# Performance work log

Measured on AMD Instinct MI355X. Metric: run time of the kernel, lower is better.

## Reference

```python
import jax, jax.numpy as jnp
import numpy as np

SPLINE_ORDER = 3
GRID_SIZE = 1
# efficient-kan style grid over [-1,1], extended by spline_order on each side; h = 2/grid_size = 2
GRID = jnp.arange(-SPLINE_ORDER, GRID_SIZE + SPLINE_ORDER + 1, dtype=jnp.float32) * 2.0 - 1.0
NB = GRID_SIZE + SPLINE_ORDER  # 4 basis functions per input feature
EPS = 1e-5


def b_splines(x, grid):
    # x: [..., in] -> [..., in, NB] via Cox-de Boor recursion
    xe = x[..., None]
    b = ((xe >= grid[:-1]) & (xe < grid[1:])).astype(x.dtype)
    for p in range(1, SPLINE_ORDER + 1):
        b = ((xe - grid[:-(p + 1)]) / (grid[p:-1] - grid[:-(p + 1)]) * b[..., :-1]
             + (grid[p + 1:] - xe) / (grid[p + 1:] - grid[1:-p]) * b[..., 1:])
    return b


def kan_linear(x, base_w, spline_w):
    # base branch: silu(x) @ W_base^T ; spline branch: B(x) contracted with W_spline [out,in,NB]
    base = jnp.einsum('...i,oi->...o', jax.nn.silu(x), base_w)
    sp = jnp.einsum('...ik,oik->...o', b_splines(x, GRID), spline_w)
    return base + sp


def kan_conv2x2(x, base_w, spline_w):
    # x: [B,C,H,W] -> [B,C_out,H-1,W-1]
    p = jax.lax.conv_general_dilated_patches(x, (2, 2), (1, 1), 'VALID')  # [B, C*4, H', W']
    p = jnp.moveaxis(p, 1, -1)  # [B,H',W',C*4]
    y = kan_linear(p, base_w, spline_w)  # [B,H',W',C_out]
    return jnp.moveaxis(y, -1, 1)


def bn2d(x, g, b):
    m = x.mean((0, 2, 3), keepdims=True)
    v = x.var((0, 2, 3), keepdims=True)
    return (x - m) * jax.lax.rsqrt(v + EPS) * g[None, :, None, None] + b[None, :, None, None]


def bn1d(x, g, b):
    m = x.mean(0, keepdims=True)
    v = x.var(0, keepdims=True)
    return (x - m) * jax.lax.rsqrt(v + EPS) * g[None, :] + b[None, :]


def maxpool2(x):
    B, C, H, W = x.shape
    Hc, Wc = (H // 2) * 2, (W // 2) * 2
    return x[:, :, :Hc, :Wc].reshape(B, C, H // 2, 2, W // 2, 2).max((3, 5))


def setup_inputs() -> dict:
    key = jax.random.key(0)
    ks = jax.random.split(key, 16)
    f32 = jnp.float32
    d = {
        'x': jax.random.normal(ks[0], (1024, 3, 32, 32), f32),
        'base_w1': jax.random.normal(ks[1], (32, 12), f32) * 0.2,
        'spline_w1': jax.random.normal(ks[2], (32, 12, NB), f32) * 0.1,
        'bn1_g': jnp.ones((32,), f32), 'bn1_b': jnp.zeros((32,), f32),
        'base_w2': jax.random.normal(ks[3], (64, 128), f32) * 0.08,
        'spline_w2': jax.random.normal(ks[4], (64, 128, NB), f32) * 0.04,
        'bn2_g': jnp.ones((64,), f32), 'bn2_b': jnp.zeros((64,), f32),
        'fc1_w': jax.random.normal(ks[5], (64, 3136), f32) * 0.02,
        'fc1_b': jnp.zeros((64,), f32),
        'bn3_g': jnp.ones((64,), f32), 'bn3_b': jnp.zeros((64,), f32),
        'fc2_w': jax.random.normal(ks[6], (10, 64), f32) * 0.1,
        'fc2_b': jnp.zeros((10,), f32),
    }
    return d


def reference(x, base_w1, spline_w1, bn1_g, bn1_b, base_w2, spline_w2, bn2_g, bn2_b,
              fc1_w, fc1_b, bn3_g, bn3_b, fc2_w, fc2_b):
    h = kan_conv2x2(x, base_w1, spline_w1)            # [B,32,31,31]
    h = jax.nn.relu(bn2d(h, bn1_g, bn1_b))
    h = maxpool2(h)                                   # [B,32,15,15]
    h = kan_conv2x2(h, base_w2, spline_w2)            # [B,64,14,14]
    h = jax.nn.relu(bn2d(h, bn2_g, bn2_b))
    h = maxpool2(h)                                   # [B,64,7,7]
    h = h.reshape(h.shape[0], -1)                     # [B,3136]
    h = h @ fc1_w.T + fc1_b
    h = jax.nn.relu(bn1d(h, bn3_g, bn3_b))
    # Dropout is identity at inference
    return h @ fc2_w.T + fc2_b                        # [B,10]
```

## Files before the change

kernel.cpp:

```cpp
#include <hip/hip_runtime.h>
#include <math.h>

#define BN_EPS 1e-5f

typedef __attribute__((ext_vector_type(8))) _Float16 f16x8;
typedef __attribute__((ext_vector_type(4))) _Float16 f16x4;
typedef __attribute__((ext_vector_type(2))) __fp16 fp16v2;
typedef __attribute__((ext_vector_type(4))) float f32x4;


__device__ __forceinline__ float siluf(float v) {
    return v * __builtin_amdgcn_rcpf(1.0f + __expf(-v));
}

__device__ __forceinline__ void expand5(float v, float f[5]) {
    f[0] = siluf(v);
    float u = (v + 7.0f) * 0.5f;
#pragma unroll
    for (int i = 0; i < 4; ++i) {
        float a = fabsf(u - (float)(i + 2));
        float p = fmaxf(2.0f - a, 0.0f);
        float q = fmaxf(1.0f - a, 0.0f);
        f[i + 1] = p * p * p - 4.0f * (q * q * q);
    }
}

__device__ __forceinline__ int pkh(float a, float b) {
    union { fp16v2 h2; int i; } u;
    u.h2 = __builtin_amdgcn_cvt_pkrtz(a, b);
    return u.i;
}


__global__ __launch_bounds__(256) void prep_kernel(
        const float* __restrict__ fw1, unsigned int* __restrict__ wTh2,
        const float* __restrict__ bw2, const float* __restrict__ sw2,
        _Float16* __restrict__ Wf,
        const float* __restrict__ bw1, const float* __restrict__ sw1,
        _Float16* __restrict__ Wf1) {
    int blk = blockIdx.x;
    if (blk < 392) {
        int t = blk * 256 + threadIdx.x;
        int o = t & 63;
        int j2 = t >> 6;
        int jc = (j2 * 2) & 63;
        int q2 = (j2 * 2) >> 6;
        wTh2[t] = (unsigned int)pkh(fw1[(size_t)o * 3136 + jc * 49 + q2],
                                    fw1[(size_t)o * 3136 + (jc + 1) * 49 + q2]);
    } else if (blk < 552) {
        int t = (blk - 392) * 256 + threadIdx.x;
        if (t >= 64 * 640) return;
        int n = t / 640;
        int k = t - n * 640;
        int s = k / 160;
        int r = k - s * 160;
        int f = r >> 5;
        int c = r & 31;
        float val = (f == 0) ? bw2[n * 128 + c * 4 + s]
                             : sw2[n * 512 + c * 16 + s * 4 + (f - 1)] * (1.0f / 6.0f);
        Wf[t] = (_Float16)val;
    } else {
        int t = (blk - 552) * 256 + threadIdx.x;
        if (t >= 32 * 64) return;
        int n = t >> 6;
        int k = t & 63;
        int s = k >> 4, j = k & 15;
        float val = 0.f;
        if (j < 15) {
            int f = j / 3, c = j - f * 3;
            int i = c * 4 + s;
            val = (f == 0) ? bw1[n * 12 + i]
                           : sw1[(n * 12 + i) * 4 + f - 1] * (1.0f / 6.0f);
        }
        Wf1[t] = (_Float16)val;
    }
}


__global__ __launch_bounds__(256, 4) void conv1_kernel(
        const float* __restrict__ x, const _Float16* __restrict__ Wf1,
        _Float16* __restrict__ pooled, float* __restrict__ part) {
    __shared__ _Float16 Eu[1025 * 16];
    __shared__ float Rs[4][64];
    char* EuB = (char*)Eu;

    int t = threadIdx.x;
    int lane = t & 63, wv = t >> 6;
    int quad = lane >> 4, l15 = lane & 15;
    int b = blockIdx.x;

    const _Float16* wb0 = Wf1 + (size_t)l15 * 64 + quad * 8;
    f16x8 bf00 = *(const f16x8*)(wb0);
    f16x8 bf01 = *(const f16x8*)(wb0 + 32);
    f16x8 bf10 = *(const f16x8*)(wb0 + 16 * 64);
    f16x8 bf11 = *(const f16x8*)(wb0 + 16 * 64 + 32);

    float xv[12];
    const float* xb = x + (size_t)b * 3072;
#pragma unroll
    for (int k = 0; k < 12; ++k) xv[k] = xb[t + k * 256];
#pragma unroll
    for (int k = 0; k < 12; ++k) {
        int idx = t + k * 256;
        int c = idx >> 10;
        int pos = idx & 1023;
        float f[5];
        expand5(xv[k], f);
        int rb = pos * 32;
        int key = (pos & 12) << 2;
        *(_Float16*)(EuB + ((rb + c * 2) ^ key))        = (_Float16)f[0];
        *(_Float16*)(EuB + ((rb + (3 + c) * 2) ^ key))  = (_Float16)f[1];
        *(_Float16*)(EuB + ((rb + (6 + c) * 2) ^ key))  = (_Float16)f[2];
        *(_Float16*)(EuB + ((rb + (9 + c) * 2) ^ key))  = (_Float16)f[3];
        *(_Float16*)(EuB + ((rb + (12 + c) * 2) ^ key)) = (_Float16)f[4];
    }
    if (t < 8) *(int*)(EuB + 32768 + t * 4) = 0;
    __syncthreads();

    int dxq = quad >> 1, hb = (quad & 1) * 16;
    int wxv = 8 * wv + (l15 & 7);
    int colb = wxv + dxq;
    int pbase = (colb * 32 + hb) ^ ((colb & 12) << 2);
    bool vx = wxv < 31;
    int pzero = 32768 + hb;
    int wy0 = l15 >> 3;

    float ss0 = 0.f, sq0 = 0.f, ss1 = 0.f, sq1 = 0.f;

    int p0 = vx ? wy0 * 1024 + pbase : pzero;
    f16x8 a0 = *(const f16x8*)(EuB + p0);
    f16x8 a1 = *(const f16x8*)(EuB + p0 + (vx ? 1024 : 0));

#pragma unroll 1
    for (int i = 0; i < 16; ++i) {
        f32x4 acc0 = (f32x4){0.f, 0.f, 0.f, 0.f};
        f32x4 acc1 = (f32x4){0.f, 0.f, 0.f, 0.f};
        acc0 = __builtin_amdgcn_mfma_f32_16x16x32_f16(a0, bf00, acc0, 0, 0, 0);
        acc1 = __builtin_amdgcn_mfma_f32_16x16x32_f16(a0, bf10, acc1, 0, 0, 0);
        acc0 = __builtin_amdgcn_mfma_f32_16x16x32_f16(a1, bf01, acc0, 0, 0, 0);
        acc1 = __builtin_amdgcn_mfma_f32_16x16x32_f16(a1, bf11, acc1, 0, 0, 0);
        if (i < 15) {
            int wyn = 2 * (i + 1) + wy0;
            bool vn = vx && (wyn < 31);
            int pn = vn ? wyn * 1024 + pbase : pzero;
            a0 = *(const f16x8*)(EuB + pn);
            a1 = *(const f16x8*)(EuB + pn + (vn ? 1024 : 0));
        }
        float h00 = fmaxf(acc0[0], acc0[1]);
        float h01 = fmaxf(acc0[2], acc0[3]);
        float h10 = fmaxf(acc1[0], acc1[1]);
        float h11 = fmaxf(acc1[2], acc1[3]);
        float g00 = fmaxf(h00, __shfl_down(h00, 32, 64));
        float g01 = fmaxf(h01, __shfl_down(h01, 32, 64));
        float g10 = fmaxf(h10, __shfl_down(h10, 32, 64));
        float g11 = fmaxf(h11, __shfl_down(h11, 32, 64));
        if (lane < 32 && i < 15) {
            int pn0 = 4 * wv + (quad & 1) * 2;
            size_t base = ((size_t)b * 225 + i * 15) * 32;
            if (pn0 < 15) {
                pooled[base + pn0 * 32 + l15]      = (_Float16)g00;
                pooled[base + pn0 * 32 + 16 + l15] = (_Float16)g10;
            }
            if (pn0 < 14) {
                pooled[base + (pn0 + 1) * 32 + l15]      = (_Float16)g01;
                pooled[base + (pn0 + 1) * 32 + 16 + l15] = (_Float16)g11;
            }
        }
        ss0 += acc0[0] + acc0[1] + acc0[2] + acc0[3];
        sq0 += acc0[0] * acc0[0] + acc0[1] * acc0[1]
             + acc0[2] * acc0[2] + acc0[3] * acc0[3];
        ss1 += acc1[0] + acc1[1] + acc1[2] + acc1[3];
        sq1 += acc1[0] * acc1[0] + acc1[1] * acc1[1]
             + acc1[2] * acc1[2] + acc1[3] * acc1[3];
    }

    ss0 += __shfl_down(ss0, 32, 64); ss0 += __shfl_down(ss0, 16, 64);
    sq0 += __shfl_down(sq0, 32, 64); sq0 += __shfl_down(sq0, 16, 64);
    ss1 += __shfl_down(ss1, 32, 64); ss1 += __shfl_down(ss1, 16, 64);
    sq1 += __shfl_down(sq1, 32, 64); sq1 += __shfl_down(sq1, 16, 64);
    if (lane < 16) {
        Rs[wv][2 * l15]          = ss0;
        Rs[wv][2 * l15 + 1]      = sq0;
        Rs[wv][32 + 2 * l15]     = ss1;
        Rs[wv][32 + 2 * l15 + 1] = sq1;
    }
    __syncthreads();
    if (t < 64)
        part[(size_t)b * 64 + t] = Rs[0][t] + Rs[1][t] + Rs[2][t] + Rs[3][t];
}


#define EU_PS 160

__device__ __forceinline__ void c2_loadb(const _Float16* __restrict__ Wb,
                                         int g, f16x8 bf[5]) {
#pragma unroll
    for (int ks = 0; ks < 5; ++ks)
        bf[ks] = *(const f16x8*)(Wb + g * 160 + ks * 32);
}

__device__ __forceinline__ void c2_mfma(const _Float16* Eu,
                                        const int abase[4][4], int g,
                                        int quad, const f16x8 bf[5],
                                        f32x4 acc[4]) {
#pragma unroll
    for (int ks = 0; ks < 5; ++ks) {
        int jo = ks * 32 + quad * 8;
#pragma unroll
        for (int mt = 0; mt < 4; ++mt) {
            f16x8 a = *(const f16x8*)&Eu[abase[mt][g] + jo];
            acc[mt] = __builtin_amdgcn_mfma_f32_16x16x32_f16(a, bf[ks], acc[mt], 0, 0, 0);
        }
    }
}

__global__ __launch_bounds__(256, 7) void conv2_kernel(
        const _Float16* __restrict__ pooled, const float* __restrict__ stats1,
        const float* __restrict__ g1v, const float* __restrict__ b1v,
        const _Float16* __restrict__ Wf, _Float16* __restrict__ Pt,
        float* __restrict__ part) {
    __shared__ _Float16 Eu[65 * EU_PS];

    int t = threadIdx.x;
    int lane = t & 63, wv = t >> 6;
    int quad = lane >> 4, l15 = lane & 15;

    int blk = blockIdx.x;
    int b = blk >> 2;
    int py0 = ((blk >> 1) & 1) * 7;
    int px0 = (blk & 1) * 7;

    const _Float16* Wb = Wf + (size_t)(wv * 16 + l15) * 640 + quad * 8;
    f16x8 bfA[5], bfB[5];
    c2_loadb(Wb, 0, bfA);

    {
        int c2 = t & 15, c0 = c2 * 2;
        int xx = (t >> 4) & 7;
        int yh = t >> 7;
        const float invN1 = 1.0f / (1024.0f * 961.0f);
        float m0 = stats1[2 * c0] * invN1;
        float v0 = stats1[2 * c0 + 1] * invN1 - m0 * m0;
        float sc0 = rsqrtf(v0 + BN_EPS) * g1v[c0];
        float sh0 = b1v[c0] - m0 * sc0;
        float m1 = stats1[2 * c0 + 2] * invN1;
        float v1 = stats1[2 * c0 + 3] * invN1 - m1 * m1;
        float sc1 = rsqrtf(v1 + BN_EPS) * g1v[c0 + 1];
        float sh1 = b1v[c0 + 1] - m1 * sc1;
        const _Float16* pbase0 =
            pooled + ((size_t)b * 225 + py0 * 15 + px0) * 32 + c0;
#pragma unroll
        for (int yi = 0; yi < 4; ++yi) {
            int yr = yh * 4 + yi;
            fp16v2 v2 = *(const fp16v2*)(pbase0 + yr * 480 + xx * 32);
            float va = fmaxf((float)v2.x * sc0 + sh0, 0.f);
            float vb = fmaxf((float)v2.y * sc1 + sh1, 0.f);
            float fa[5], fb5[5];
            expand5(va, fa);
            expand5(vb, fb5);
            int* eb = (int*)&Eu[(yr * 8 + xx) * EU_PS] + c2;
            eb[0]  = pkh(fa[0], fb5[0]);
            eb[16] = pkh(fa[1], fb5[1]);
            eb[32] = pkh(fa[2], fb5[2]);
            eb[48] = pkh(fa[3], fb5[3]);
            eb[64] = pkh(fa[4], fb5[4]);
        }
    }
    if (t < 80) ((int*)&Eu[64 * EU_PS])[t] = 0;

    int abase[4][4];
#pragma unroll
    for (int mt = 0; mt < 4; ++mt) {
        int m = mt * 16 + l15;
        if (m < 49) {
            int pr = m / 7, pc = m - pr * 7;
#pragma unroll
            for (int s = 0; s < 4; ++s)
                abase[mt][s] = ((pr + (s >> 1)) * 8 + pc + (s & 1)) * EU_PS;
        } else {
#pragma unroll
            for (int s = 0; s < 4; ++s) abase[mt][s] = 64 * EU_PS;
        }
    }
    __syncthreads();

    f32x4 acc[4];
#pragma unroll
    for (int mt = 0; mt < 4; ++mt) acc[mt] = (f32x4){0.f, 0.f, 0.f, 0.f};

    c2_loadb(Wb, 1, bfB);
    c2_mfma(Eu, abase, 0, quad, bfA, acc);
    c2_loadb(Wb, 2, bfA);
    c2_mfma(Eu, abase, 1, quad, bfB, acc);
    c2_loadb(Wb, 3, bfB);
    c2_mfma(Eu, abase, 2, quad, bfA, acc);
    c2_mfma(Eu, abase, 3, quad, bfB, acc);

    int o = wv * 16 + l15;
#pragma unroll
    for (int mt = 0; mt < 4; ++mt) {
#pragma unroll
        for (int reg = 0; reg < 4; ++reg) {
            int m = mt * 16 + quad * 4 + reg;
            if (m < 49) {
                int pr = m / 7, pc = m - pr * 7;
                int patch = (b * 14 + py0 + pr) * 14 + px0 + pc;
                Pt[(size_t)patch * 64 + o] = (_Float16)acc[mt][reg];
            }
        }
    }
    float s = 0.f, s2 = 0.f;
#pragma unroll
    for (int mt = 0; mt < 4; ++mt)
#pragma unroll
        for (int reg = 0; reg < 4; ++reg) {
            float a = acc[mt][reg];
            s += a;
            s2 += a * a;
        }
    s  += __shfl_down(s, 16, 64);  s  += __shfl_down(s, 32, 64);
    s2 += __shfl_down(s2, 16, 64); s2 += __shfl_down(s2, 32, 64);
    if (lane < 16) {
        part[(size_t)blk * 128 + 2 * o]     = s;
        part[(size_t)blk * 128 + 2 * o + 1] = s2;
    }
}


__global__ __launch_bounds__(256) void redstats_kernel(
        const float* __restrict__ part, float* __restrict__ stats,
        int nblk, int stride) {
    int p = blockIdx.x;
    float s = 0.f;
    for (int j = threadIdx.x; j < nblk; j += 256)
        s += part[(size_t)j * stride + p];
#pragma unroll
    for (int off = 32; off > 0; off >>= 1) s += __shfl_down(s, off, 64);
    __shared__ float ls[4];
    if ((threadIdx.x & 63) == 0) ls[threadIdx.x >> 6] = s;
    __syncthreads();
    if (threadIdx.x == 0) stats[p] = ls[0] + ls[1] + ls[2] + ls[3];
}


__global__ __launch_bounds__(256) void bnpool2_kernel(
        const _Float16* __restrict__ Pt, const float* __restrict__ stats,
        const float* __restrict__ g, const float* __restrict__ bb,
        _Float16* __restrict__ out) {
    int t = blockIdx.x * 256 + threadIdx.x;
    if (t >= 1024 * 49 * 16) return;
    int c4 = (t & 15) * 4;
    int q2 = (t >> 4) % 49;
    int b  = t / (49 * 16);
    float sc[4], sh[4];
#pragma unroll
    for (int j = 0; j < 4; ++j) {
        int c = c4 + j;
        float mean = stats[2 * c] * (1.0f / 200704.0f);
        float var  = stats[2 * c + 1] * (1.0f / 200704.0f) - mean * mean;
        sc[j] = rsqrtf(var + BN_EPS) * g[c];
        sh[j] = bb[c] - mean * sc[j];
    }
    int py2 = q2 / 7, px2 = q2 - py2 * 7;
    int q = (py2 * 2) * 14 + px2 * 2;
    const _Float16* p = Pt + ((size_t)b * 196 + q) * 64 + c4;
    f16x4 r0 = *(const f16x4*)(p);
    f16x4 r1 = *(const f16x4*)(p + 64);
    f16x4 r2 = *(const f16x4*)(p + 14 * 64);
    f16x4 r3 = *(const f16x4*)(p + 15 * 64);
    f16x4 res;
#pragma unroll
    for (int j = 0; j < 4; ++j) {
        float v0 = fmaxf((float)r0[j] * sc[j] + sh[j], 0.f);
        float v1 = fmaxf((float)r1[j] * sc[j] + sh[j], 0.f);
        float v2 = fmaxf((float)r2[j] * sc[j] + sh[j], 0.f);
        float v3 = fmaxf((float)r3[j] * sc[j] + sh[j], 0.f);
        res[j] = (_Float16)fmaxf(fmaxf(v0, v1), fmaxf(v2, v3));
    }
    *(f16x4*)(out + (size_t)b * 3136 + q2 * 64 + c4) = res;
}


__global__ __launch_bounds__(256) void fc1_kernel(
        const _Float16* __restrict__ xin, const unsigned int* __restrict__ wTh2,
        const float* __restrict__ bias, float* __restrict__ z) {
    __shared__ unsigned int xsu[2 * 1568];
    __shared__ float red[2][4][64];
    int b0 = blockIdx.x * 2;
    const unsigned int* xg = (const unsigned int*)xin + (size_t)b0 * 1568;
    for (int j = threadIdx.x; j < 2 * 1568; j += 256) xsu[j] = xg[j];
    __syncthreads();
    int o = threadIdx.x & 63, q = threadIdx.x >> 6;
    float s0 = 0.f, s1 = 0.f;
    const unsigned int* wp = wTh2 + (size_t)q * 392 * 64 + o;
    int jb = q * 392;
    for (int i = 0; i < 392; ++i) {
        union { unsigned int u; fp16v2 h; } uw, u0, u1;
        uw.u = wp[i * 64];
        u0.u = xsu[jb + i];
        u1.u = xsu[1568 + jb + i];
        s0 = __builtin_amdgcn_fdot2(u0.h, uw.h, s0, false);
        s1 = __builtin_amdgcn_fdot2(u1.h, uw.h, s1, false);
    }
    red[0][q][o] = s0; red[1][q][o] = s1;
    __syncthreads();
    if (threadIdx.x < 128) {
        int bb = threadIdx.x >> 6;
        int oo = threadIdx.x & 63;
        float tot = red[bb][0][oo] + red[bb][1][oo] + red[bb][2][oo]
                  + red[bb][3][oo] + bias[oo];
        z[((size_t)(b0 + bb)) * 64 + oo] = tot;
    }
}


__global__ __launch_bounds__(256) void colstats_kernel(
        const float* __restrict__ z, const float* __restrict__ g,
        const float* __restrict__ bb, float* __restrict__ scsh) {
    int c = blockIdx.x;
    float s = 0.f, s2 = 0.f;
    for (int b = threadIdx.x; b < 1024; b += 256) {
        float v = z[(size_t)b * 64 + c];
        s += v; s2 += v * v;
    }
#pragma unroll
    for (int off = 32; off > 0; off >>= 1) {
        s  += __shfl_down(s, off, 64);
        s2 += __shfl_down(s2, off, 64);
    }
    __shared__ float ls[8];
    int w = threadIdx.x >> 6;
    if ((threadIdx.x & 63) == 0) { ls[w * 2] = s; ls[w * 2 + 1] = s2; }
    __syncthreads();
    if (threadIdx.x == 0) {
        float st = ls[0] + ls[2] + ls[4] + ls[6];
        float st2 = ls[1] + ls[3] + ls[5] + ls[7];
        float mean = st * (1.0f / 1024.0f);
        float var  = st2 * (1.0f / 1024.0f) - mean * mean;
        float sc = rsqrtf(var + BN_EPS) * g[c];
        scsh[2 * c]     = sc;
        scsh[2 * c + 1] = bb[c] - mean * sc;
    }
}


__global__ __launch_bounds__(256) void final_kernel(
        const float* __restrict__ z, const float* __restrict__ scsh,
        const float* __restrict__ w2, const float* __restrict__ b2,
        float* __restrict__ out) {
    int t = blockIdx.x * 256 + threadIdx.x;
    if (t >= 10240) return;
    int o = t % 10, b = t / 10;
    float acc = b2[o];
#pragma unroll 8
    for (int c = 0; c < 64; ++c) {
        float a = fmaxf(z[(size_t)b * 64 + c] * scsh[2 * c] + scsh[2 * c + 1], 0.f);
        acc += a * w2[o * 64 + c];
    }
    out[t] = acc;
}


extern "C" void kernel_launch(void* const* d_in, const int* in_sizes, int n_in,
                              void* d_out, int out_size, void* d_ws, size_t ws_size,
                              hipStream_t stream) {
    const float* x   = (const float*)d_in[0];
    const float* bw1 = (const float*)d_in[1];
    const float* sw1 = (const float*)d_in[2];
    const float* g1  = (const float*)d_in[3];
    const float* b1  = (const float*)d_in[4];
    const float* bw2 = (const float*)d_in[5];
    const float* sw2 = (const float*)d_in[6];
    const float* g2  = (const float*)d_in[7];
    const float* b2v = (const float*)d_in[8];
    const float* fw1 = (const float*)d_in[9];
    const float* fb1 = (const float*)d_in[10];
    const float* g3  = (const float*)d_in[11];
    const float* b3  = (const float*)d_in[12];
    const float* fw2 = (const float*)d_in[13];
    const float* fb2 = (const float*)d_in[14];
    float* out = (float*)d_out;

    char* ws = (char*)d_ws;
    float* part1     = (float*)(ws);
    _Float16* Pt     = (_Float16*)(ws);
    float* part2     = (float*)(ws + 51380224);
    _Float16* Wf     = (_Float16*)(ws + 100000000);
    _Float16* Wf1    = (_Float16*)(ws + 100131072);
    _Float16* pooled = (_Float16*)(ws + 125960192);
    float* z         = (float*)(ws + 155451392);
    unsigned int* wTh2 = (unsigned int*)(ws + 155713536);
    float* stats1    = (float*)(ws + 156516352);
    float* stats2    = (float*)(ws + 156516608);
    float* stats3    = (float*)(ws + 156517120);

    prep_kernel<<<560, 256, 0, stream>>>(fw1, wTh2, bw2, sw2, Wf, bw1, sw1, Wf1);

    conv1_kernel<<<1024, 256, 0, stream>>>(x, Wf1, pooled, part1);
    redstats_kernel<<<64, 256, 0, stream>>>(part1, stats1, 1024, 64);

    conv2_kernel<<<4096, 256, 0, stream>>>(pooled, stats1, g1, b1,
                                           Wf, Pt, part2);
    redstats_kernel<<<128, 256, 0, stream>>>(part2, stats2, 4096, 128);

    _Float16* pooled2 = pooled;
    bnpool2_kernel<<<(1024 * 49 * 16 + 255) / 256, 256, 0, stream>>>(
        Pt, stats2, g2, b2v, pooled2);

    fc1_kernel<<<512, 256, 0, stream>>>(pooled2, wTh2, fb1, z);
    colstats_kernel<<<64, 256, 0, stream>>>(z, g3, b3, stats3);
    final_kernel<<<(10240 + 255) / 256, 256, 0, stream>>>(z, stats3, fw2, fb2, out);
}
```

Baseline: 190.5 us.

## Fuse BN2+pool into fc1 and replace conv1 stat reduction with atomics

Folds the batchnorm-2 normalize, ReLU and 2x2 maxpool into the fc1 kernel's shared-memory staging step, so the separate bnpool2 kernel and its pooled fp16 round trip through global memory go away. The conv1 per-block statistics are now accumulated directly into stats1 with atomicAdd, and the prep kernel zeroes stats1 first, which removes the redstats launch for stage 1. This cuts two launches and some traffic, at the cost of 1024 blocks contending on 64 atomic floats and a non-deterministic summation order. Dead v0/v1 computations are left in the fused loop.

Result: slower. 201.8 us (+6.0%).

```diff
diff --git a/kernel.cpp b/kernel.cpp
--- a/kernel.cpp
+++ b/kernel.cpp
@@ -37,7 +37,7 @@
         const float* __restrict__ bw2, const float* __restrict__ sw2,
         _Float16* __restrict__ Wf,
         const float* __restrict__ bw1, const float* __restrict__ sw1,
-        _Float16* __restrict__ Wf1) {
+        _Float16* __restrict__ Wf1, float* __restrict__ stats1) {
     int blk = blockIdx.x;
     if (blk < 392) {
         int t = blk * 256 + threadIdx.x;
@@ -60,7 +60,9 @@
                              : sw2[n * 512 + c * 16 + s * 4 + (f - 1)] * (1.0f / 6.0f);
         Wf[t] = (_Float16)val;
     } else {
-        int t = (blk - 552) * 256 + threadIdx.x;
+        int tid = threadIdx.x;
+        if (blk == 559 && tid < 64) stats1[tid] = 0.f;
+        int t = (blk - 552) * 256 + tid;
         if (t >= 32 * 64) return;
         int n = t >> 6;
         int k = t & 63;
@@ -79,7 +81,7 @@
 
 __global__ __launch_bounds__(256, 4) void conv1_kernel(
         const float* __restrict__ x, const _Float16* __restrict__ Wf1,
-        _Float16* __restrict__ pooled, float* __restrict__ part) {
+        _Float16* __restrict__ pooled, float* __restrict__ stats1) {
     __shared__ _Float16 Eu[1025 * 16];
     __shared__ float Rs[4][64];
     char* EuB = (char*)Eu;
@@ -186,7 +188,7 @@
     }
     __syncthreads();
     if (t < 64)
-        part[(size_t)b * 64 + t] = Rs[0][t] + Rs[1][t] + Rs[2][t] + Rs[3][t];
+        atomicAdd(&stats1[t], Rs[0][t] + Rs[1][t] + Rs[2][t] + Rs[3][t]);
 }
 
 
@@ -343,57 +345,54 @@
 }
 
 
-__global__ __launch_bounds__(256) void bnpool2_kernel(
+__global__ __launch_bounds__(256) void fc1_kernel(
         const _Float16* __restrict__ Pt, const float* __restrict__ stats,
         const float* __restrict__ g, const float* __restrict__ bb,
-        _Float16* __restrict__ out) {
-    int t = blockIdx.x * 256 + threadIdx.x;
-    if (t >= 1024 * 49 * 16) return;
-    int c4 = (t & 15) * 4;
-    int q2 = (t >> 4) % 49;
-    int b  = t / (49 * 16);
-    float sc[4], sh[4];
-#pragma unroll
-    for (int j = 0; j < 4; ++j) {
-        int c = c4 + j;
-        float mean = stats[2 * c] * (1.0f / 200704.0f);
-        float var  = stats[2 * c + 1] * (1.0f / 200704.0f) - mean * mean;
-        sc[j] = rsqrtf(var + BN_EPS) * g[c];
-        sh[j] = bb[c] - mean * sc[j];
-    }
-    int py2 = q2 / 7, px2 = q2 - py2 * 7;
-    int q = (py2 * 2) * 14 + px2 * 2;
-    const _Float16* p = Pt + ((size_t)b * 196 + q) * 64 + c4;
-    f16x4 r0 = *(const f16x4*)(p);
-    f16x4 r1 = *(const f16x4*)(p + 64);
-    f16x4 r2 = *(const f16x4*)(p + 14 * 64);
-    f16x4 r3 = *(const f16x4*)(p + 15 * 64);
-    f16x4 res;
-#pragma unroll
-    for (int j = 0; j < 4; ++j) {
-        float v0 = fmaxf((float)r0[j] * sc[j] + sh[j], 0.f);
-        float v1 = fmaxf((float)r1[j] * sc[j] + sh[j], 0.f);
-        float v2 = fmaxf((float)r2[j] * sc[j] + sh[j], 0.f);
-        float v3 = fmaxf((float)r3[j] * sc[j] + sh[j], 0.f);
-        res[j] = (_Float16)fmaxf(fmaxf(v0, v1), fmaxf(v2, v3));
-    }
-    *(f16x4*)(out + (size_t)b * 3136 + q2 * 64 + c4) = res;
-}
-
-
-__global__ __launch_bounds__(256) void fc1_kernel(
-        const _Float16* __restrict__ xin, const unsigned int* __restrict__ wTh2,
-        const float* __restrict__ bias, float* __restrict__ z) {
+        const unsigned int* __restrict__ wTh2, const float* __restrict__ bias,
+        float* __restrict__ z) {
     __shared__ unsigned int xsu[2 * 1568];
     __shared__ float red[2][4][64];
+    __shared__ float scs[64], shs[64];
+    int t = threadIdx.x;
     int b0 = blockIdx.x * 2;
-    const unsigned int* xg = (const unsigned int*)xin + (size_t)b0 * 1568;
-    for (int j = threadIdx.x; j < 2 * 1568; j += 256) xsu[j] = xg[j];
-    __syncthreads();
-    int o = threadIdx.x & 63, q = threadIdx.x >> 6;
+    if (t < 64) {
+        float mean = stats[2 * t] * (1.0f / 200704.0f);
+        float var  = stats[2 * t + 1] * (1.0f / 200704.0f) - mean * mean;
+        float sc = rsqrtf(var + BN_EPS) * g[t];
+        scs[t] = sc;
+        shs[t] = bb[t] - mean * sc;
+    }
+    __syncthreads();
+    for (int task = t; task < 3136; task += 256) {
+        int img = task / 1568;
+        int r = task - img * 1568;
+        int q2 = r >> 5, c2 = r & 31;
+        int c0 = c2 * 2;
+        int py2 = q2 / 7, px2 = q2 - py2 * 7;
+        int q = (py2 * 2) * 14 + px2 * 2;
+        const _Float16* p = Pt + ((size_t)(b0 + img) * 196 + q) * 64 + c0;
+        fp16v2 r0 = *(const fp16v2*)(p);
+        fp16v2 r1 = *(const fp16v2*)(p + 64);
+        fp16v2 r2 = *(const fp16v2*)(p + 14 * 64);
+        fp16v2 r3 = *(const fp16v2*)(p + 15 * 64);
+        float sc0 = scs[c0], sh0 = shs[c0];
+        float sc1 = scs[c0 + 1], sh1 = shs[c0 + 1];
+        float v0 = fmaxf(fmaxf((float)r0.x, (float)r1.x),
+                         fmaxf((float)r2.x, (float)r3.x)) * sc0 + sh0;
+        float v1 = fmaxf(fmaxf((float)r0.y, (float)r1.y),
+                         fmaxf((float)r2.y, (float)r3.y)) * sc1 + sh1;
+        float w0 = fmaxf(fmaxf((float)r0.x * sc0 + sh0, (float)r1.x * sc0 + sh0),
+                         fmaxf((float)r2.x * sc0 + sh0, (float)r3.x * sc0 + sh0));
+        float w1 = fmaxf(fmaxf((float)r0.y * sc1 + sh1, (float)r1.y * sc1 + sh1),
+                         fmaxf((float)r2.y * sc1 + sh1, (float)r3.y * sc1 + sh1));
+        (void)v0; (void)v1;
+        xsu[task] = (unsigned int)pkh(fmaxf(w0, 0.f), fmaxf(w1, 0.f));
+    }
+    __syncthreads();
+    int o = t & 63, qq = t >> 6;
     float s0 = 0.f, s1 = 0.f;
-    const unsigned int* wp = wTh2 + (size_t)q * 392 * 64 + o;
-    int jb = q * 392;
+    const unsigned int* wp = wTh2 + (size_t)qq * 392 * 64 + o;
+    int jb = qq * 392;
     for (int i = 0; i < 392; ++i) {
         union { unsigned int u; fp16v2 h; } uw, u0, u1;
         uw.u = wp[i * 64];
@@ -402,14 +401,14 @@
         s0 = __builtin_amdgcn_fdot2(u0.h, uw.h, s0, false);
         s1 = __builtin_amdgcn_fdot2(u1.h, uw.h, s1, false);
     }
-    red[0][q][o] = s0; red[1][q][o] = s1;
-    __syncthreads();
-    if (threadIdx.x < 128) {
-        int bb = threadIdx.x >> 6;
-        int oo = threadIdx.x & 63;
-        float tot = red[bb][0][oo] + red[bb][1][oo] + red[bb][2][oo]
-                  + red[bb][3][oo] + bias[oo];
-        z[((size_t)(b0 + bb)) * 64 + oo] = tot;
+    red[0][qq][o] = s0; red[1][qq][o] = s1;
+    __syncthreads();
+    if (t < 128) {
+        int bb2 = t >> 6;
+        int oo = t & 63;
+        float tot = red[bb2][0][oo] + red[bb2][1][oo] + red[bb2][2][oo]
+                  + red[bb2][3][oo] + bias[oo];
+        z[((size_t)(b0 + bb2)) * 64 + oo] = tot;
     }
 }
 
@@ -482,7 +481,6 @@
     float* out = (float*)d_out;
 
     char* ws = (char*)d_ws;
-    float* part1     = (float*)(ws);
     _Float16* Pt     = (_Float16*)(ws);
     float* part2     = (float*)(ws + 51380224);
     _Float16* Wf     = (_Float16*)(ws + 100000000);
@@ -494,20 +492,16 @@
     float* stats2    = (float*)(ws + 156516608);
     float* stats3    = (float*)(ws + 156517120);
 
-    prep_kernel<<<560, 256, 0, stream>>>(fw1, wTh2, bw2, sw2, Wf, bw1, sw1, Wf1);
-
-    conv1_kernel<<<1024, 256, 0, stream>>>(x, Wf1, pooled, part1);
-    redstats_kernel<<<64, 256, 0, stream>>>(part1, stats1, 1024, 64);
+    prep_kernel<<<560, 256, 0, stream>>>(fw1, wTh2, bw2, sw2, Wf, bw1, sw1, Wf1,
+                                         stats1);
+
+    conv1_kernel<<<1024, 256, 0, stream>>>(x, Wf1, pooled, stats1);
 
     conv2_kernel<<<4096, 256, 0, stream>>>(pooled, stats1, g1, b1,
                                            Wf, Pt, part2);
     redstats_kernel<<<128, 256, 0, stream>>>(part2, stats2, 4096, 128);
 
-    _Float16* pooled2 = pooled;
-    bnpool2_kernel<<<(1024 * 49 * 16 + 255) / 256, 256, 0, stream>>>(
-        Pt, stats2, g2, b2v, pooled2);
-
-    fc1_kernel<<<512, 256, 0, stream>>>(pooled2, wTh2, fb1, z);
+    fc1_kernel<<<512, 256, 0, stream>>>(Pt, stats2, g2, b2v, wTh2, fb1, z);
     colstats_kernel<<<64, 256, 0, stream>>>(z, g3, b3, stats3);
     final_kernel<<<(10240 + 255) / 256, 256, 0, stream>>>(z, stats3, fw2, fb2, out);
 }
```
